# Optimization experiments

Hardware: AMD Instinct MI355X
Metric: run time of the kernel (lower is better)

Reference implementation:

```python
import jax, jax.numpy as jnp
import numpy as np

B, N, F = 128, 4096, 32
E, H, DEPTH, OUT = 16, 7, 3, 2
EH = E * H


def _ln(x, g, b, eps=1e-6):
    m = jnp.mean(x, axis=-1, keepdims=True)
    v = jnp.mean(jnp.square(x - m), axis=-1, keepdims=True)
    return (x - m) / jnp.sqrt(v + eps) * g + b


def setup_inputs() -> dict:
    key = jax.random.key(0)
    ks = jax.random.split(key, 24)
    s = 0.05
    inp = {
        "X": jax.random.normal(ks[0], (B, N, F), jnp.float32),
        "avail": jax.random.randint(ks[1], (B, N), 0, 2, jnp.int32),
        "W_enc1": jax.random.normal(ks[2], (F, E), jnp.float32) * s,
        "b_enc1": jnp.zeros((E,), jnp.float32),
        "W_enc2": jax.random.normal(ks[3], (E, E), jnp.float32) * s,
        "b_enc2": jnp.zeros((E,), jnp.float32),
        "W_enc3": jax.random.normal(ks[4], (E, E), jnp.float32) * s,
        "b_enc3": jnp.zeros((E,), jnp.float32),
        "g_enc": jnp.ones((E,), jnp.float32),
        "be_enc": jnp.zeros((E,), jnp.float32),
        "W_agg": jax.random.normal(ks[5], (DEPTH, E, H), jnp.float32) * s,
        "b_agg": jnp.zeros((DEPTH, H), jnp.float32),
        "W_phi1": jax.random.normal(ks[6], (DEPTH, E, EH), jnp.float32) * s,
        "b_phi1": jnp.zeros((DEPTH, EH), jnp.float32),
        "W_phi2": jax.random.normal(ks[7], (DEPTH, EH, EH), jnp.float32) * s,
        "b_phi2": jnp.zeros((DEPTH, EH), jnp.float32),
        "g_phi": jnp.ones((DEPTH, EH), jnp.float32),
        "be_phi": jnp.zeros((DEPTH, EH), jnp.float32),
        "W_proj": jax.random.normal(ks[8], (E, OUT), jnp.float32) * s,
        "b_proj": jnp.zeros((OUT,), jnp.float32),
    }
    return inp


def reference(X, avail, W_enc1, b_enc1, W_enc2, b_enc2, W_enc3, b_enc3, g_enc, be_enc,
              W_agg, b_agg, W_phi1, b_phi1, W_phi2, b_phi2, g_phi, be_phi, W_proj, b_proj):
    # init encoder: Dense-relu, Dense-relu, Dense, LayerNorm  -> Z: [B, N, E]
    Z = jax.nn.relu(X @ W_enc1 + b_enc1)
    Z = jax.nn.relu(Z @ W_enc2 + b_enc2)
    Z = Z @ W_enc3 + b_enc3
    Z = _ln(Z, g_enc, be_enc)
    X_embd = Z

    af = avail.astype(Z.dtype)                      # [B, N]
    num_avail = jnp.maximum(jnp.sum(af, axis=1), 1.0)  # [B]

    for d in range(DEPTH):
        # block_type='qua': fc(Z^2) -> [B, N, H]
        fcZ = jnp.square(Z) @ W_agg[d] + b_agg[d]
        # masked mean over the set axis -> Zbar: [B, H]
        Zbar = jnp.einsum('bnh,bn->bh', fcZ, af) / num_avail[:, None]
        # NonlinearMap(X_embd): Dense-relu-Dense-LayerNorm -> [B, N, E*H]
        phi = jax.nn.relu(X_embd @ W_phi1[d] + b_phi1[d])
        phi = phi @ W_phi2[d] + b_phi2[d]
        phi = _ln(phi, g_phi[d], be_phi[d])
        phi_rs = phi.reshape(phi.shape[0], phi.shape[1], H, E)  # [B, N, H, E]
        # delta = mean_h(phi_rs * Zbar[:,None,:,None]) -> [B, N, E]
        delta = jnp.einsum('bnhe,bh->bne', phi_rs, Zbar) / H
        Z = Z + delta

    return Z @ W_proj + b_proj  # [B, N, OUT]
```

## Files before the change

kernel.cpp:

```cpp
#include <hip/hip_runtime.h>
#include <hip/hip_bf16.h>

#define Bb 128
#define Nn 4096
#define Ff 32
#define Ee 16
#define Hh 7
#define EH 112
#define NROW (Bb*Nn)
#define PS 136
#define NBLK 2048

typedef __attribute__((ext_vector_type(8))) short  bf16x8;
typedef __attribute__((ext_vector_type(4))) float  f32x4;
typedef __attribute__((ext_vector_type(4))) unsigned int u32x4;
typedef __attribute__((ext_vector_type(2))) unsigned int u32x2;

__device__ inline unsigned pack2(float a, float b) {
    __hip_bfloat162 h = __float22bfloat162_rn(make_float2(a, b));
    return *reinterpret_cast<unsigned*>(&h);
}
union BF8 { unsigned u[4]; bf16x8 v; u32x4 q; };

__global__ __launch_bounds__(256) void enc_kernel(
    const float* __restrict__ X,
    const float* __restrict__ W1, const float* __restrict__ b1,
    const float* __restrict__ W2, const float* __restrict__ b2,
    const float* __restrict__ W3, const float* __restrict__ b3,
    const float* __restrict__ g,  const float* __restrict__ be,
    const float* __restrict__ Wagg0, const int* __restrict__ avail,
    unsigned short* __restrict__ XeBF, float* __restrict__ acc0)
{
    __shared__ float sW1[Ff*Ee], sW2[Ee*Ee], sW3[Ee*Ee];
    __shared__ float sb1[Ee], sb2[Ee], sb3[Ee], sg[Ee], sbe[Ee];
    __shared__ float sWq[Ee*Hh];
    __shared__ float red[256][8];
    int tid = threadIdx.x;
    for (int i = tid; i < Ff*Ee; i += 256) sW1[i] = W1[i];
    for (int i = tid; i < Ee*Ee; i += 256) { sW2[i] = W2[i]; sW3[i] = W3[i]; }
    if (tid < Ee) { sb1[tid]=b1[tid]; sb2[tid]=b2[tid]; sb3[tid]=b3[tid];
                    sg[tid]=g[tid];   sbe[tid]=be[tid]; }
    if (tid < Ee*Hh) sWq[tid] = Wagg0[tid];
    __syncthreads();

    size_t row = (size_t)blockIdx.x * 256u + (unsigned)tid;
    const float4* xr = reinterpret_cast<const float4*>(X + row * Ff);
    float x[Ff];
    #pragma unroll
    for (int i = 0; i < Ff/4; ++i) {
        float4 v = xr[i];
        x[4*i+0]=v.x; x[4*i+1]=v.y; x[4*i+2]=v.z; x[4*i+3]=v.w;
    }
    float h1[Ee];
    #pragma unroll
    for (int e = 0; e < Ee; ++e) h1[e] = sb1[e];
    #pragma unroll 4
    for (int k = 0; k < Ff; ++k) {
        float xk = x[k];
        #pragma unroll
        for (int e = 0; e < Ee; ++e) h1[e] = fmaf(xk, sW1[k*Ee+e], h1[e]);
    }
    #pragma unroll
    for (int e = 0; e < Ee; ++e) h1[e] = fmaxf(h1[e], 0.f);

    float h2[Ee];
    #pragma unroll
    for (int e = 0; e < Ee; ++e) h2[e] = sb2[e];
    #pragma unroll 4
    for (int k = 0; k < Ee; ++k) {
        float hk = h1[k];
        #pragma unroll
        for (int e = 0; e < Ee; ++e) h2[e] = fmaf(hk, sW2[k*Ee+e], h2[e]);
    }
    #pragma unroll
    for (int e = 0; e < Ee; ++e) h2[e] = fmaxf(h2[e], 0.f);

    float z[Ee];
    #pragma unroll
    for (int e = 0; e < Ee; ++e) z[e] = sb3[e];
    #pragma unroll 4
    for (int k = 0; k < Ee; ++k) {
        float hk = h2[k];
        #pragma unroll
        for (int e = 0; e < Ee; ++e) z[e] = fmaf(hk, sW3[k*Ee+e], z[e]);
    }
    float m = 0.f;
    #pragma unroll
    for (int e = 0; e < Ee; ++e) m += z[e];
    m *= (1.f/Ee);
    float v = 0.f;
    #pragma unroll
    for (int e = 0; e < Ee; ++e) { float d = z[e]-m; v += d*d; }
    v *= (1.f/Ee);
    float inv = rsqrtf(v + 1e-6f);
    #pragma unroll
    for (int e = 0; e < Ee; ++e) z[e] = (z[e]-m)*inv*sg[e] + sbe[e];

    unsigned us[8];
    #pragma unroll
    for (int j = 0; j < 8; ++j) us[j] = pack2(z[2*j], z[2*j+1]);
    u32x4 lo = {us[0],us[1],us[2],us[3]};
    u32x4 hi = {us[4],us[5],us[6],us[7]};
    u32x4* xo = reinterpret_cast<u32x4*>(XeBF + row*Ee);
    xo[0] = lo; xo[1] = hi;

    float af = (float)avail[row];
    float fc[Hh];
    #pragma unroll
    for (int h = 0; h < Hh; ++h) fc[h] = 0.f;
    #pragma unroll
    for (int e = 0; e < Ee; ++e) {
        float z2 = z[e]*z[e];
        #pragma unroll
        for (int h = 0; h < Hh; ++h) fc[h] = fmaf(z2, sWq[e*Hh+h], fc[h]);
    }
    #pragma unroll
    for (int h = 0; h < Hh; ++h) red[tid][h] = af * fc[h];
    red[tid][7] = af;
    __syncthreads();
    for (int s = 128; s > 0; s >>= 1) {
        if (tid < s) {
            #pragma unroll
            for (int q2 = 0; q2 < 8; ++q2) red[tid][q2] += red[tid+s][q2];
        }
        __syncthreads();
    }
    if (tid < 8) atomicAdd(&acc0[(blockIdx.x >> 4)*8 + tid], red[0][tid]);
}

__global__ __launch_bounds__(256) void wpack(
    const float* __restrict__ W_phi2, const float* __restrict__ W_phi1,
    const float* __restrict__ b_phi1, const float* __restrict__ b_phi2,
    unsigned short* __restrict__ W2F, unsigned short* __restrict__ W1F)
{
    int idx = blockIdx.x*256 + threadIdx.x;
    if (idx < 3*28*64) {
        int d = idx / (28*64); int r = idx % (28*64);
        int f = r >> 6, l = r & 63;
        int lg = l >> 4, li = l & 15, mt = f >> 2, kt = f & 3;
        const float* W2g = W_phi2 + (size_t)d*EH*EH;
        const float* b2g = b_phi2 + (size_t)d*EH;
        int mm = mt*16 + li;
        unsigned v[4];
        #pragma unroll
        for (int jj = 0; jj < 4; ++jj) {
            int k0 = kt*32 + lg*8 + jj*2;
            float a = (k0 < EH) ? W2g[(size_t)k0*EH + mm]
                                : (k0 == EH ? b2g[mm] : 0.f);
            float c = (k0+1 < EH) ? W2g[(size_t)(k0+1)*EH + mm] : 0.f;
            v[jj] = pack2(a, c);
        }
        u32x4 q = {v[0], v[1], v[2], v[3]};
        *reinterpret_cast<u32x4*>(W2F + (size_t)idx*8) = q;
    } else if (idx < 3*28*64 + 3*7*64) {
        int r2 = idx - 3*28*64;
        int d = r2 / (7*64); int r = r2 % (7*64);
        int mt = r >> 6, l = r & 63;
        int g = l >> 4, i = l & 15;
        const float* W1g = W_phi1 + (size_t)d*Ee*EH;
        const float* b1g = b_phi1 + (size_t)d*EH;
        int mm = mt*16 + i;
        unsigned v[4];
        #pragma unroll
        for (int jj = 0; jj < 4; ++jj) {
            float a = 0.f, c = 0.f;
            if (g < 2) {
                a = W1g[(size_t)(g*8 + jj*2)  *EH + mm];
                c = W1g[(size_t)(g*8 + jj*2+1)*EH + mm];
            } else if (g == 2 && jj == 0) {
                a = b1g[mm];
            }
            v[jj] = pack2(a, c);
        }
        u32x4 q = {v[0], v[1], v[2], v[3]};
        *reinterpret_cast<u32x4*>(W1F + (size_t)r2*8) = q;
    }
}

template<bool LAST>
__global__ __launch_bounds__(256, 2) void phi_mfma(
    const unsigned short* __restrict__ Zin,
    const unsigned short* __restrict__ Xe,
    unsigned short* __restrict__ Zout,
    const float* __restrict__ accIn, const float* __restrict__ baggD,
    const float* __restrict__ WaggN, float* __restrict__ accN,
    const int* __restrict__ avail,
    const unsigned short* __restrict__ W1F,
    const unsigned short* __restrict__ W2F,
    const float* __restrict__ gg,  const float* __restrict__ beg,
    const float* __restrict__ Wp,  const float* __restrict__ bp,
    float* __restrict__ out)
{
    __shared__ __align__(16) unsigned short sW2F[28*512];
    __shared__ __align__(16) unsigned short sP1[4][2][16*PS];
    __shared__ float sRed[4][8];

    int tid  = threadIdx.x;
    int wave = tid >> 6, lane = tid & 63;
    int g = lane >> 4, i = lane & 15;

    for (int p = tid; p < 28*64; p += 256)
        *reinterpret_cast<u32x4*>(&sW2F[p*8]) =
            *reinterpret_cast<const u32x4*>(W2F + (size_t)p*8);
    for (int p = tid; p < (4*2*16*PS)/8; p += 256) {
        u32x4 zq = {0u,0u,0u,0u};
        reinterpret_cast<u32x4*>(&sP1[0][0][0])[p] = zq;
    }
    __syncthreads();
    if (tid < 128) {
        int w = tid >> 5, bb = (tid >> 4) & 1, r = tid & 15;
        sP1[w][bb][r*PS + 112] = 0x3F80;
    }

    int b = blockIdx.x >> 4;
    float cntb = accIn[b*8 + 7];
    float cden = fmaxf(cntb, 1.f);
    float zb[Hh];
    #pragma unroll
    for (int h = 0; h < Hh; ++h)
        zb[h] = (accIn[b*8 + h] + baggD[h]*cntb) / cden * (1.f/Hh);

    f32x4 gz[7];
    float Gz[4] = {0,0,0,0}, Bz[4] = {0,0,0,0};
    #pragma unroll
    for (int mt = 0; mt < 7; ++mt) {
        f32x4 pg = *reinterpret_cast<const f32x4*>(gg  + mt*16 + 4*g);
        f32x4 pe = *reinterpret_cast<const f32x4*>(beg + mt*16 + 4*g);
        #pragma unroll
        for (int r = 0; r < 4; ++r) {
            float gzv = pg[r] * zb[mt];
            gz[mt][r] = gzv;
            Gz[r] += gzv;
            Bz[r] += pe[r] * zb[mt];
        }
    }
    bf16x8 aW1[7];
    #pragma unroll
    for (int mt = 0; mt < 7; ++mt)
        aW1[mt] = *reinterpret_cast<const bf16x8*>(W1F + (size_t)(mt*64 + lane)*8);

    f32x4 wq[7];
    if (!LAST) {
        #pragma unroll
        for (int h = 0; h < Hh; ++h)
            #pragma unroll
            for (int r = 0; r < 4; ++r)
                wq[h][r] = WaggN[(4*g + r)*Hh + h];
    }
    float wpa[4] = {0,0,0,0}, wpb[4] = {0,0,0,0}, bp0 = 0.f, bp1 = 0.f;
    if (LAST) {
        f32x4 u0 = *reinterpret_cast<const f32x4*>(Wp + 8*g);
        f32x4 u1 = *reinterpret_cast<const f32x4*>(Wp + 8*g + 4);
        wpa[0]=u0[0]; wpa[1]=u0[2]; wpa[2]=u1[0]; wpa[3]=u1[2];
        wpb[0]=u0[1]; wpb[1]=u0[3]; wpb[2]=u1[1]; wpb[3]=u1[3];
        bp0 = bp[0]; bp1 = bp[1];
    }
    float wacc[Hh] = {0,0,0,0,0,0,0};
    float wcnt = 0.f;
    __syncthreads();

    size_t r0 = (size_t)(blockIdx.x*16 + wave*4) * 16;

    BF8 bz_; bz_.u[0]=bz_.u[1]=bz_.u[2]=bz_.u[3]=0u;
    if (g == 2) bz_.u[0] = 0x00003F80u;
    bf16x8 bx0 = bz_.v, bx1 = bz_.v, bx2 = bz_.v, bx3 = bz_.v;
    if (g < 2) {
        const unsigned short* xp = Xe + (r0 + i)*Ee + g*8;
        bx0 = *reinterpret_cast<const bf16x8*>(xp);
        bx1 = *reinterpret_cast<const bf16x8*>(xp + 16*Ee);
        bx2 = *reinterpret_cast<const bf16x8*>(xp + 32*Ee);
        bx3 = *reinterpret_cast<const bf16x8*>(xp + 48*Ee);
    }
    const unsigned short* zp = Zin + (r0 + i)*Ee + 4*g;
    u32x2 zu0 = *reinterpret_cast<const u32x2*>(zp);
    u32x2 zu1 = *reinterpret_cast<const u32x2*>(zp + 16*Ee);
    u32x2 zu2 = *reinterpret_cast<const u32x2*>(zp + 32*Ee);
    u32x2 zu3 = *reinterpret_cast<const u32x2*>(zp + 48*Ee);

    unsigned short* p1A = &sP1[wave][0][0];
    unsigned short* p1B = &sP1[wave][1][0];
    const f32x4 zz = {0.f,0.f,0.f,0.f};

    auto epi = [&](const f32x4* d2, u32x2 zu, size_t row0) {
        float s = 0.f;
        #pragma unroll
        for (int mt = 0; mt < 7; ++mt) s += d2[mt][0]+d2[mt][1]+d2[mt][2]+d2[mt][3];
        s += __shfl_xor(s, 16); s += __shfl_xor(s, 32);
        float m = s * (1.f/EH);
        float q = 0.f;
        #pragma unroll
        for (int mt = 0; mt < 7; ++mt) {
            #pragma unroll
            for (int r = 0; r < 4; ++r) { float dd = d2[mt][r]-m; q = fmaf(dd,dd,q); }
        }
        q += __shfl_xor(q, 16); q += __shfl_xor(q, 32);
        float inv = rsqrtf(q*(1.f/EH) + 1e-6f);

        float S1[4] = {0,0,0,0};
        #pragma unroll
        for (int mt = 0; mt < 7; ++mt) {
            #pragma unroll
            for (int r = 0; r < 4; ++r) S1[r] = fmaf(d2[mt][r], gz[mt][r], S1[r]);
        }
        unsigned lo = zu[0], hi = zu[1];
        float zv[4];
        zv[0] = __uint_as_float((lo & 0xFFFFu) << 16);
        zv[1] = __uint_as_float(lo & 0xFFFF0000u);
        zv[2] = __uint_as_float((hi & 0xFFFFu) << 16);
        zv[3] = __uint_as_float(hi & 0xFFFF0000u);
        float zn[4];
        #pragma unroll
        for (int r = 0; r < 4; ++r)
            zn[r] = zv[r] + (fmaf(-m, Gz[r], S1[r]) * inv + Bz[r]);

        if (!LAST) {
            u32x2 w = {pack2(zn[0], zn[1]), pack2(zn[2], zn[3])};
            *reinterpret_cast<u32x2*>(Zout + (row0 + i)*Ee + 4*g) = w;
            float af = (float)avail[row0 + i];
            float z20 = zn[0]*zn[0], z21 = zn[1]*zn[1];
            float z22 = zn[2]*zn[2], z23 = zn[3]*zn[3];
            #pragma unroll
            for (int h = 0; h < Hh; ++h) {
                float f = z20*wq[h][0] + z21*wq[h][1] + z22*wq[h][2] + z23*wq[h][3];
                f += __shfl_xor(f, 16); f += __shfl_xor(f, 32);
                wacc[h] = fmaf(af, f, wacc[h]);
            }
            wcnt += af;
        } else {
            float o0 = zn[0]*wpa[0] + zn[1]*wpa[1] + zn[2]*wpa[2] + zn[3]*wpa[3];
            float o1 = zn[0]*wpb[0] + zn[1]*wpb[1] + zn[2]*wpb[2] + zn[3]*wpb[3];
            o0 += __shfl_xor(o0, 16); o0 += __shfl_xor(o0, 32);
            o1 += __shfl_xor(o1, 16); o1 += __shfl_xor(o1, 32);
            if (g == 0) {
                float2 o; o.x = o0 + bp0; o.y = o1 + bp1;
                *reinterpret_cast<float2*>(out + (row0 + i)*2) = o;
            }
        }
    };

    auto pair = [&](bf16x8 bxA, bf16x8 bxB, u32x2 zuA, u32x2 zuB, size_t rowA) {
        #pragma unroll
        for (int mt = 0; mt < 7; ++mt) {
            f32x4 dA = __builtin_amdgcn_mfma_f32_16x16x32_bf16(aW1[mt], bxA, zz, 0,0,0);
            f32x4 dB = __builtin_amdgcn_mfma_f32_16x16x32_bf16(aW1[mt], bxB, zz, 0,0,0);
            #pragma unroll
            for (int r = 0; r < 4; ++r) { dA[r] = fmaxf(dA[r],0.f); dB[r] = fmaxf(dB[r],0.f); }
            u32x2 wA = {pack2(dA[0],dA[1]), pack2(dA[2],dA[3])};
            u32x2 wB = {pack2(dB[0],dB[1]), pack2(dB[2],dB[3])};
            *reinterpret_cast<u32x2*>(&p1A[i*PS + mt*16 + 4*g]) = wA;
            *reinterpret_cast<u32x2*>(&p1B[i*PS + mt*16 + 4*g]) = wB;
        }
        f32x4 d2A[7], d2B[7];
        #pragma unroll
        for (int mt = 0; mt < 7; ++mt) { d2A[mt] = zz; d2B[mt] = zz; }
        #pragma unroll
        for (int kt = 0; kt < 4; ++kt) {
            bf16x8 bpA = *reinterpret_cast<const bf16x8*>(&p1A[i*PS + kt*32 + 8*g]);
            bf16x8 bpB = *reinterpret_cast<const bf16x8*>(&p1B[i*PS + kt*32 + 8*g]);
            #pragma unroll
            for (int mt = 0; mt < 7; ++mt) {
                bf16x8 a = *reinterpret_cast<const bf16x8*>(&sW2F[(mt*4 + kt)*512 + lane*8]);
                d2A[mt] = __builtin_amdgcn_mfma_f32_16x16x32_bf16(a, bpA, d2A[mt], 0,0,0);
                d2B[mt] = __builtin_amdgcn_mfma_f32_16x16x32_bf16(a, bpB, d2B[mt], 0,0,0);
            }
        }
        epi(d2A, zuA, rowA);
        epi(d2B, zuB, rowA + 16);
    };

    pair(bx0, bx1, zu0, zu1, r0);
    pair(bx2, bx3, zu2, zu3, r0 + 32);

    if (!LAST) {
        #pragma unroll
        for (int off = 1; off < 64; off <<= 1) {
            #pragma unroll
            for (int h = 0; h < Hh; ++h) wacc[h] += __shfl_xor(wacc[h], off);
            wcnt += __shfl_xor(wcnt, off);
        }
        if (lane == 0) {
            #pragma unroll
            for (int h = 0; h < Hh; ++h) sRed[wave][h] = wacc[h]*0.25f;
            sRed[wave][7] = wcnt*0.25f;
        }
        __syncthreads();
        if (tid < 8)
            atomicAdd(&accN[b*8 + tid],
                      sRed[0][tid]+sRed[1][tid]+sRed[2][tid]+sRed[3][tid]);
    }
}

extern "C" void kernel_launch(void* const* d_in, const int* in_sizes, int n_in,
                              void* d_out, int out_size, void* d_ws, size_t ws_size,
                              hipStream_t stream)
{
    const float* X      = (const float*)d_in[0];
    const int*   avail  = (const int*)  d_in[1];
    const float* W_enc1 = (const float*)d_in[2];  const float* b_enc1 = (const float*)d_in[3];
    const float* W_enc2 = (const float*)d_in[4];  const float* b_enc2 = (const float*)d_in[5];
    const float* W_enc3 = (const float*)d_in[6];  const float* b_enc3 = (const float*)d_in[7];
    const float* g_enc  = (const float*)d_in[8];  const float* be_enc = (const float*)d_in[9];
    const float* W_agg  = (const float*)d_in[10]; const float* b_agg  = (const float*)d_in[11];
    const float* W_phi1 = (const float*)d_in[12]; const float* b_phi1 = (const float*)d_in[13];
    const float* W_phi2 = (const float*)d_in[14]; const float* b_phi2 = (const float*)d_in[15];
    const float* g_phi  = (const float*)d_in[16]; const float* be_phi = (const float*)d_in[17];
    const float* W_proj = (const float*)d_in[18]; const float* b_proj = (const float*)d_in[19];
    float* out = (float*)d_out;

    char* ws = (char*)d_ws;
    unsigned short* XeBF = (unsigned short*)ws;
    unsigned short* Zb   = (unsigned short*)(ws + (size_t)NROW*Ee*2);
    char* p = ws + 2*(size_t)NROW*Ee*2;
    float* acc = (float*)p;                  p += 3*Bb*8*sizeof(float);
    unsigned short* W2F = (unsigned short*)p; p += (size_t)3*28*512*2;
    unsigned short* W1F = (unsigned short*)p;

    hipMemsetAsync(acc, 0, 3*Bb*8*sizeof(float), stream);
    wpack<<<(3*28*64 + 3*7*64 + 255)/256, 256, 0, stream>>>(
        W_phi2, W_phi1, b_phi1, b_phi2, W2F, W1F);

    enc_kernel<<<NBLK, 256, 0, stream>>>(
        X, W_enc1, b_enc1, W_enc2, b_enc2, W_enc3, b_enc3, g_enc, be_enc,
        W_agg, avail, XeBF, acc);

    phi_mfma<false><<<NBLK, 256, 0, stream>>>(
        XeBF, XeBF, Zb, acc, b_agg, W_agg + Ee*Hh, acc + Bb*8, avail,
        W1F, W2F, g_phi, be_phi, W_proj, b_proj, out);

    phi_mfma<false><<<NBLK, 256, 0, stream>>>(
        Zb, XeBF, Zb, acc + Bb*8, b_agg + Hh, W_agg + 2*Ee*Hh, acc + 2*Bb*8, avail,
        W1F + (size_t)7*512, W2F + (size_t)28*512,
        g_phi + EH, be_phi + EH, W_proj, b_proj, out);

    phi_mfma<true><<<NBLK, 256, 0, stream>>>(
        Zb, XeBF, Zb, acc + 2*Bb*8, b_agg + 2*Hh, W_agg, acc, avail,
        W1F + (size_t)14*512, W2F + (size_t)56*512,
        g_phi + 2*EH, be_phi + 2*EH, W_proj, b_proj, out);
}
```

Measured before the change: 167.9 us.

## Raise phi kernel occupancy: drop W2 LDS staging, swizzle P1, defer aggregation

Measured after the change: 342.2 us. +103.9%, slower.

```diff
diff --git a/kernel.cpp b/kernel.cpp
--- a/kernel.cpp
+++ b/kernel.cpp
@@ -8,7 +8,6 @@
 #define Hh 7
 #define EH 112
 #define NROW (Bb*Nn)
-#define PS 136
 #define NBLK 2048
 
 typedef __attribute__((ext_vector_type(8))) short  bf16x8;
@@ -178,7 +177,7 @@
 }
 
 template<bool LAST>
-__global__ __launch_bounds__(256, 2) void phi_mfma(
+__global__ __launch_bounds__(256, 4) void phi_mfma(
     const unsigned short* __restrict__ Zin,
     const unsigned short* __restrict__ Xe,
     unsigned short* __restrict__ Zout,
@@ -191,25 +190,17 @@
     const float* __restrict__ Wp,  const float* __restrict__ bp,
     float* __restrict__ out)
 {
-    __shared__ __align__(16) unsigned short sW2F[28*512];
-    __shared__ __align__(16) unsigned short sP1[4][2][16*PS];
-    __shared__ float sRed[4][8];
+    __shared__ __align__(16) unsigned short sP1[4][2][16*128];
+    __shared__ __align__(16) float sGZ[EH];
 
     int tid  = threadIdx.x;
     int wave = tid >> 6, lane = tid & 63;
     int g = lane >> 4, i = lane & 15;
-
-    for (int p = tid; p < 28*64; p += 256)
-        *reinterpret_cast<u32x4*>(&sW2F[p*8]) =
-            *reinterpret_cast<const u32x4*>(W2F + (size_t)p*8);
-    for (int p = tid; p < (4*2*16*PS)/8; p += 256) {
+    int i7 = i & 7;
+
+    for (int p = tid; p < (4*2*16*128)/8; p += 256) {
         u32x4 zq = {0u,0u,0u,0u};
         reinterpret_cast<u32x4*>(&sP1[0][0][0])[p] = zq;
-    }
-    __syncthreads();
-    if (tid < 128) {
-        int w = tid >> 5, bb = (tid >> 4) & 1, r = tid & 15;
-        sP1[w][bb][r*PS + 112] = 0x3F80;
     }
 
     int b = blockIdx.x >> 4;
@@ -219,33 +210,22 @@
     #pragma unroll
     for (int h = 0; h < Hh; ++h)
         zb[h] = (accIn[b*8 + h] + baggD[h]*cntb) / cden * (1.f/Hh);
-
-    f32x4 gz[7];
+    if (tid < EH) sGZ[tid] = gg[tid] * zb[tid >> 4];
+    __syncthreads();
+
+    if (g == 0) {
+        int idx = i*128 + ((14 ^ i7) << 3);
+        sP1[wave][0][idx] = 0x3F80;
+        sP1[wave][1][idx] = 0x3F80;
+    }
+
     float Gz[4] = {0,0,0,0}, Bz[4] = {0,0,0,0};
     #pragma unroll
     for (int mt = 0; mt < 7; ++mt) {
-        f32x4 pg = *reinterpret_cast<const f32x4*>(gg  + mt*16 + 4*g);
-        f32x4 pe = *reinterpret_cast<const f32x4*>(beg + mt*16 + 4*g);
-        #pragma unroll
-        for (int r = 0; r < 4; ++r) {
-            float gzv = pg[r] * zb[mt];
-            gz[mt][r] = gzv;
-            Gz[r] += gzv;
-            Bz[r] += pe[r] * zb[mt];
-        }
-    }
-    bf16x8 aW1[7];
-    #pragma unroll
-    for (int mt = 0; mt < 7; ++mt)
-        aW1[mt] = *reinterpret_cast<const bf16x8*>(W1F + (size_t)(mt*64 + lane)*8);
-
-    f32x4 wq[7];
-    if (!LAST) {
-        #pragma unroll
-        for (int h = 0; h < Hh; ++h)
-            #pragma unroll
-            for (int r = 0; r < 4; ++r)
-                wq[h][r] = WaggN[(4*g + r)*Hh + h];
+        f32x4 gv = *reinterpret_cast<const f32x4*>(&sGZ[mt*16 + 4*g]);
+        f32x4 bv = *reinterpret_cast<const f32x4*>(beg + mt*16 + 4*g);
+        #pragma unroll
+        for (int r = 0; r < 4; ++r) { Gz[r] += gv[r]; Bz[r] += bv[r]*zb[mt]; }
     }
     float wpa[4] = {0,0,0,0}, wpb[4] = {0,0,0,0}, bp0 = 0.f, bp1 = 0.f;
     if (LAST) {
@@ -255,53 +235,36 @@
         wpb[0]=u0[1]; wpb[1]=u0[3]; wpb[2]=u1[1]; wpb[3]=u1[3];
         bp0 = bp[0]; bp1 = bp[1];
     }
-    float wacc[Hh] = {0,0,0,0,0,0,0};
+    float wacc2[4] = {0,0,0,0};
     float wcnt = 0.f;
-    __syncthreads();
 
     size_t r0 = (size_t)(blockIdx.x*16 + wave*4) * 16;
-
-    BF8 bz_; bz_.u[0]=bz_.u[1]=bz_.u[2]=bz_.u[3]=0u;
-    if (g == 2) bz_.u[0] = 0x00003F80u;
-    bf16x8 bx0 = bz_.v, bx1 = bz_.v, bx2 = bz_.v, bx3 = bz_.v;
-    if (g < 2) {
-        const unsigned short* xp = Xe + (r0 + i)*Ee + g*8;
-        bx0 = *reinterpret_cast<const bf16x8*>(xp);
-        bx1 = *reinterpret_cast<const bf16x8*>(xp + 16*Ee);
-        bx2 = *reinterpret_cast<const bf16x8*>(xp + 32*Ee);
-        bx3 = *reinterpret_cast<const bf16x8*>(xp + 48*Ee);
-    }
-    const unsigned short* zp = Zin + (r0 + i)*Ee + 4*g;
-    u32x2 zu0 = *reinterpret_cast<const u32x2*>(zp);
-    u32x2 zu1 = *reinterpret_cast<const u32x2*>(zp + 16*Ee);
-    u32x2 zu2 = *reinterpret_cast<const u32x2*>(zp + 32*Ee);
-    u32x2 zu3 = *reinterpret_cast<const u32x2*>(zp + 48*Ee);
-
     unsigned short* p1A = &sP1[wave][0][0];
     unsigned short* p1B = &sP1[wave][1][0];
     const f32x4 zz = {0.f,0.f,0.f,0.f};
 
-    auto epi = [&](const f32x4* d2, u32x2 zu, size_t row0) {
-        float s = 0.f;
-        #pragma unroll
-        for (int mt = 0; mt < 7; ++mt) s += d2[mt][0]+d2[mt][1]+d2[mt][2]+d2[mt][3];
-        s += __shfl_xor(s, 16); s += __shfl_xor(s, 32);
+    auto epi = [&](const f32x4 (&d2)[7], size_t row0, float af) {
+        float s = 0.f, q = 0.f;
+        #pragma unroll
+        for (int mt = 0; mt < 7; ++mt) {
+            #pragma unroll
+            for (int r = 0; r < 4; ++r) { float v = d2[mt][r]; s += v; q = fmaf(v,v,q); }
+        }
+        s += __shfl_xor(s, 16); q += __shfl_xor(q, 16);
+        s += __shfl_xor(s, 32); q += __shfl_xor(q, 32);
         float m = s * (1.f/EH);
-        float q = 0.f;
+        float var = fmaf(-m, m, q * (1.f/EH));
+        float inv = rsqrtf(var + 1e-6f);
+
+        float S1[4] = {0,0,0,0};
         #pragma unroll
         for (int mt = 0; mt < 7; ++mt) {
-            #pragma unroll
-            for (int r = 0; r < 4; ++r) { float dd = d2[mt][r]-m; q = fmaf(dd,dd,q); }
-        }
-        q += __shfl_xor(q, 16); q += __shfl_xor(q, 32);
-        float inv = rsqrtf(q*(1.f/EH) + 1e-6f);
-
-        float S1[4] = {0,0,0,0};
-        #pragma unroll
-        for (int mt = 0; mt < 7; ++mt) {
-            #pragma unroll
-            for (int r = 0; r < 4; ++r) S1[r] = fmaf(d2[mt][r], gz[mt][r], S1[r]);
-        }
+            f32x4 gv = *reinterpret_cast<const f32x4*>(&sGZ[mt*16 + 4*g]);
+            #pragma unroll
+            for (int r = 0; r < 4; ++r) S1[r] = fmaf(d2[mt][r], gv[r], S1[r]);
+        }
+        u32x2 zu = __builtin_nontemporal_load(
+            reinterpret_cast<const u32x2*>(Zin + (row0 + i)*Ee + 4*g));
         unsigned lo = zu[0], hi = zu[1];
         float zv[4];
         zv[0] = __uint_as_float((lo & 0xFFFFu) << 16);
@@ -311,20 +274,13 @@
         float zn[4];
         #pragma unroll
         for (int r = 0; r < 4; ++r)
-            zn[r] = zv[r] + (fmaf(-m, Gz[r], S1[r]) * inv + Bz[r]);
+            zn[r] = zv[r] + fmaf(-m, Gz[r], S1[r]) * inv + Bz[r];
 
         if (!LAST) {
             u32x2 w = {pack2(zn[0], zn[1]), pack2(zn[2], zn[3])};
             *reinterpret_cast<u32x2*>(Zout + (row0 + i)*Ee + 4*g) = w;
-            float af = (float)avail[row0 + i];
-            float z20 = zn[0]*zn[0], z21 = zn[1]*zn[1];
-            float z22 = zn[2]*zn[2], z23 = zn[3]*zn[3];
-            #pragma unroll
-            for (int h = 0; h < Hh; ++h) {
-                float f = z20*wq[h][0] + z21*wq[h][1] + z22*wq[h][2] + z23*wq[h][3];
-                f += __shfl_xor(f, 16); f += __shfl_xor(f, 32);
-                wacc[h] = fmaf(af, f, wacc[h]);
-            }
+            #pragma unroll
+            for (int r = 0; r < 4; ++r) wacc2[r] = fmaf(af, zn[r]*zn[r], wacc2[r]);
             wcnt += af;
         } else {
             float o0 = zn[0]*wpa[0] + zn[1]*wpa[1] + zn[2]*wpa[2] + zn[3]*wpa[3];
@@ -338,7 +294,25 @@
         }
     };
 
-    auto pair = [&](bf16x8 bxA, bf16x8 bxB, u32x2 zuA, u32x2 zuB, size_t rowA) {
+    auto pair = [&](size_t rowA) {
+        BF8 bz_; bz_.u[0]=bz_.u[1]=bz_.u[2]=bz_.u[3]=0u;
+        if (g == 2) bz_.u[0] = 0x00003F80u;
+        bf16x8 bxA = bz_.v, bxB = bz_.v;
+        if (g < 2) {
+            bxA = __builtin_nontemporal_load(
+                reinterpret_cast<const bf16x8*>(Xe + (rowA + i)*Ee + g*8));
+            bxB = __builtin_nontemporal_load(
+                reinterpret_cast<const bf16x8*>(Xe + (rowA + 16 + i)*Ee + g*8));
+        }
+        float afA = 0.f, afB = 0.f;
+        if (!LAST) {
+            afA = (float)__builtin_nontemporal_load(avail + rowA + i);
+            afB = (float)__builtin_nontemporal_load(avail + rowA + 16 + i);
+        }
+        bf16x8 aW1[7];
+        #pragma unroll
+        for (int mt = 0; mt < 7; ++mt)
+            aW1[mt] = *reinterpret_cast<const bf16x8*>(W1F + (size_t)(mt*64 + lane)*8);
         #pragma unroll
         for (int mt = 0; mt < 7; ++mt) {
             f32x4 dA = __builtin_amdgcn_mfma_f32_16x16x32_bf16(aW1[mt], bxA, zz, 0,0,0);
@@ -347,46 +321,54 @@
             for (int r = 0; r < 4; ++r) { dA[r] = fmaxf(dA[r],0.f); dB[r] = fmaxf(dB[r],0.f); }
             u32x2 wA = {pack2(dA[0],dA[1]), pack2(dA[2],dA[3])};
             u32x2 wB = {pack2(dB[0],dB[1]), pack2(dB[2],dB[3])};
-            *reinterpret_cast<u32x2*>(&p1A[i*PS + mt*16 + 4*g]) = wA;
-            *reinterpret_cast<u32x2*>(&p1B[i*PS + mt*16 + 4*g]) = wB;
+            int widx = i*128 + (((2*mt + (g>>1)) ^ i7) << 3) + ((g&1) << 2);
+            *reinterpret_cast<u32x2*>(&p1A[widx]) = wA;
+            *reinterpret_cast<u32x2*>(&p1B[widx]) = wB;
         }
         f32x4 d2A[7], d2B[7];
         #pragma unroll
         for (int mt = 0; mt < 7; ++mt) { d2A[mt] = zz; d2B[mt] = zz; }
         #pragma unroll
         for (int kt = 0; kt < 4; ++kt) {
-            bf16x8 bpA = *reinterpret_cast<const bf16x8*>(&p1A[i*PS + kt*32 + 8*g]);
-            bf16x8 bpB = *reinterpret_cast<const bf16x8*>(&p1B[i*PS + kt*32 + 8*g]);
+            int ridx = i*128 + (((4*kt + g) ^ i7) << 3);
+            bf16x8 bpA = *reinterpret_cast<const bf16x8*>(&p1A[ridx]);
+            bf16x8 bpB = *reinterpret_cast<const bf16x8*>(&p1B[ridx]);
             #pragma unroll
             for (int mt = 0; mt < 7; ++mt) {
-                bf16x8 a = *reinterpret_cast<const bf16x8*>(&sW2F[(mt*4 + kt)*512 + lane*8]);
+                bf16x8 a = *reinterpret_cast<const bf16x8*>(
+                    W2F + (size_t)((mt*4 + kt)*64 + lane)*8);
                 d2A[mt] = __builtin_amdgcn_mfma_f32_16x16x32_bf16(a, bpA, d2A[mt], 0,0,0);
                 d2B[mt] = __builtin_amdgcn_mfma_f32_16x16x32_bf16(a, bpB, d2B[mt], 0,0,0);
             }
         }
-        epi(d2A, zuA, rowA);
-        epi(d2B, zuB, rowA + 16);
+        epi(d2A, rowA, afA);
+        epi(d2B, rowA + 16, afB);
     };
 
-    pair(bx0, bx1, zu0, zu1, r0);
-    pair(bx2, bx3, zu2, zu3, r0 + 32);
+    pair(r0);
+    pair(r0 + 32);
 
     if (!LAST) {
+        float f[Hh];
+        #pragma unroll
+        for (int h = 0; h < Hh; ++h) {
+            float a = 0.f;
+            #pragma unroll
+            for (int r = 0; r < 4; ++r)
+                a = fmaf(WaggN[(4*g + r)*Hh + h], wacc2[r], a);
+            f[h] = a;
+        }
         #pragma unroll
         for (int off = 1; off < 64; off <<= 1) {
             #pragma unroll
-            for (int h = 0; h < Hh; ++h) wacc[h] += __shfl_xor(wacc[h], off);
+            for (int h = 0; h < Hh; ++h) f[h] += __shfl_xor(f[h], off);
             wcnt += __shfl_xor(wcnt, off);
         }
         if (lane == 0) {
             #pragma unroll
-            for (int h = 0; h < Hh; ++h) sRed[wave][h] = wacc[h]*0.25f;
-            sRed[wave][7] = wcnt*0.25f;
-        }
-        __syncthreads();
-        if (tid < 8)
-            atomicAdd(&accN[b*8 + tid],
-                      sRed[0][tid]+sRed[1][tid]+sRed[2][tid]+sRed[3][tid]);
+            for (int h = 0; h < Hh; ++h) atomicAdd(&accN[b*8 + h], f[h]);
+            atomicAdd(&accN[b*8 + 7], wcnt * 0.25f);
+        }
     }
 }
 
```
